# Optimization experiments

Measured on AMD Instinct MI355X. Metric: run time of the kernel, lower is better.

The kernel has to match this reference:

```python
import jax, jax.numpy as jnp
import numpy as np

N = 50000      # nodes
E = 800000     # edges (before self-loops)
IN_DIM = 256
HID = 32       # per-head hidden of conv1
OUT = 8        # per-head out of conv2 (mean over heads)
H = 4          # heads


def setup_inputs() -> dict:
    key = jax.random.key(0)
    k = jax.random.split(key, 8)
    x = jax.random.normal(k[0], (N, IN_DIM), dtype=jnp.float32)
    src = jax.random.randint(k[1], (E,), 0, N)
    dst = jax.random.randint(k[2], (E,), 0, N)
    # emulate remove_self_loops: perturb any accidental self-loop
    dst = jnp.where(src == dst, (dst + 1) % N, dst)
    edge_index = jnp.stack([src, dst])
    sc1 = 1.0 / np.sqrt(IN_DIM)
    W1 = jax.random.uniform(k[3], (IN_DIM, H * HID), jnp.float32, -sc1, sc1)
    att1 = jax.random.uniform(k[4], (H, HID), jnp.float32, -0.1, 0.1)
    b1 = jnp.zeros((H * HID,), jnp.float32)
    sc2 = 1.0 / np.sqrt(H * HID)
    W2 = jax.random.uniform(k[5], (H * HID, H * OUT), jnp.float32, -sc2, sc2)
    att2 = jax.random.uniform(k[6], (H, OUT), jnp.float32, -0.1, 0.1)
    b2 = jnp.zeros((OUT,), jnp.float32)
    return {"x": x, "edge_index": edge_index, "W1": W1, "att1": att1,
            "b1": b1, "W2": W2, "att2": att2, "b2": b2}


def _segment_softmax(logits, seg, num_segments):
    # logits: [E, H], seg: [E] destination ids. Every segment is non-empty
    # (self-loops added), so no -inf survives.
    m = jnp.full((num_segments, logits.shape[1]), -jnp.inf, logits.dtype)
    m = m.at[seg].max(logits)
    e = jnp.exp(logits - m[seg])
    z = jax.ops.segment_sum(e, seg, num_segments=num_segments)
    return e / (z[seg] + 1e-16)


def _oodgat_conv(x, W, att, bias, src, dst, concat):
    n = x.shape[0]
    h = (x @ W).reshape(n, att.shape[0], att.shape[1])          # [N, H, C]
    s = jax.nn.sigmoid(jnp.einsum('nhc,hc->nh', h, att))        # [N, H] node scores
    si, sj = s[dst], s[src]                                      # [E, H]
    # OODGAT similarity weight (adjust=True): agree-in-distribution term
    logits = si * sj + (1.0 - si) * (1.0 - sj)
    alpha = _segment_softmax(logits, dst, n)                     # [E, H]
    msg = h[src] * alpha[:, :, None]                             # [E, H, C]
    out = jax.ops.segment_sum(msg, dst, num_segments=n)          # [N, H, C]
    out = out.reshape(n, -1) if concat else out.mean(axis=1)
    return out + bias


def reference(x, edge_index, W1, att1, b1, W2, att2, b2):
    n = x.shape[0]
    loop = jnp.arange(n)
    src = jnp.concatenate([edge_index[0], loop])  # add_self_loops
    dst = jnp.concatenate([edge_index[1], loop])
    # eval mode: dropout (drop_input/drop_prob/drop_edge) are identity
    h = jax.nn.elu(_oodgat_conv(x, W1, att1, b1, src, dst, True))
    return _oodgat_conv(h, W2, att2, b2, src, dst, False)
```

## Files before the change

kernel.cpp:

```cpp
#include <hip/hip_runtime.h>
#include <math.h>


typedef __attribute__((ext_vector_type(8))) short bf16x8;
typedef __attribute__((ext_vector_type(4))) float f32x4;

__device__ inline ushort f2bf(float f) {
    uint u = __float_as_uint(f);
    return (ushort)((u + 0x7fffu + ((u >> 16) & 1u)) >> 16);
}
__device__ inline float bf_lo(uint u) { return __uint_as_float(u << 16); }
__device__ inline float bf_hi(uint u) { return __uint_as_float(u & 0xffff0000u); }


__global__ void count_pos_k(const int* __restrict__ dstA, int E, int ET,
                            int* __restrict__ deg, ushort* __restrict__ epos) {
    int e = blockIdx.x * blockDim.x + threadIdx.x;
    if (e >= ET) return;
    int d = (e < E) ? dstA[e] : (e - E);
    epos[e] = (ushort)atomicAdd(&deg[d], 1);
}

__global__ __launch_bounds__(256) void scan_a_k(const int* __restrict__ deg, int n,
                                                int* __restrict__ rowstart,
                                                int* __restrict__ bsum) {
    __shared__ int ts[256];
    int t = threadIdx.x;
    int idx = blockIdx.x * 1024 + t * 4;
    int4 v = make_int4(0, 0, 0, 0);
    if (idx + 3 < n) {
        v = *(const int4*)(deg + idx);
    } else {
        if (idx < n)     v.x = deg[idx];
        if (idx + 1 < n) v.y = deg[idx + 1];
        if (idx + 2 < n) v.z = deg[idx + 2];
        if (idx + 3 < n) v.w = deg[idx + 3];
    }
    int s = v.x + v.y + v.z + v.w;
    ts[t] = s;
    __syncthreads();
#pragma unroll
    for (int off = 1; off < 256; off <<= 1) {
        int u = (t >= off) ? ts[t - off] : 0;
        __syncthreads();
        ts[t] += u;
        __syncthreads();
    }
    int excl = ts[t] - s;
    int p1 = excl + v.x, p2 = p1 + v.y, p3 = p2 + v.z;
    if (idx < n)     rowstart[idx]     = excl;
    if (idx + 1 < n) rowstart[idx + 1] = p1;
    if (idx + 2 < n) rowstart[idx + 2] = p2;
    if (idx + 3 < n) rowstart[idx + 3] = p3;
    if (t == 255) bsum[blockIdx.x] = ts[255];
}

__global__ __launch_bounds__(256) void scan_b_k(const int* __restrict__ bsum, int nb,
                                                int* __restrict__ boff,
                                                int* __restrict__ totalp) {
    __shared__ int ts[256];
    int t = threadIdx.x;
    int v = (t < nb) ? bsum[t] : 0;
    ts[t] = v;
    __syncthreads();
#pragma unroll
    for (int off = 1; off < 256; off <<= 1) {
        int u = (t >= off) ? ts[t - off] : 0;
        __syncthreads();
        ts[t] += u;
        __syncthreads();
    }
    if (t < nb) boff[t] = ts[t] - v;
    if (t == nb - 1) *totalp = ts[t];
}

__global__ void scan_c_k(int* __restrict__ rowstart, const int* __restrict__ boff,
                         int n) {
    int i = blockIdx.x * blockDim.x + threadIdx.x;
    if (i < n) rowstart[i] += boff[i >> 10];
}

__global__ void scatter_k(const int* __restrict__ srcA, const int* __restrict__ dstA,
                          int E, int ET, const int* __restrict__ rowstart,
                          const ushort* __restrict__ epos,
                          ushort* __restrict__ csrc) {
    int e = blockIdx.x * blockDim.x + threadIdx.x;
    if (e >= ET) return;
    int d, s;
    if (e < E) { d = dstA[e]; s = srcA[e]; } else { d = e - E; s = e - E; }
    csrc[rowstart[d] + epos[e]] = (ushort)s;
}


__global__ void prep_wt_k(const float* __restrict__ W, ushort* __restrict__ Wt) {
    int idx = blockIdx.x * blockDim.x + threadIdx.x;
    if (idx >= 256 * 128) return;
    int k = idx >> 7, col = idx & 127;
    Wt[col * 256 + k] = f2bf(W[idx]);
}


__global__ __launch_bounds__(256) void gemm1_k(const float* __restrict__ X,
                                               const ushort* __restrict__ Wt,
                                               const float* __restrict__ ATT1,
                                               uint* __restrict__ H1b,
                                               float* __restrict__ S1, int n) {
    __shared__ __align__(16) ushort Alds[4][128][8];
    __shared__ __align__(16) ushort Blds[4][128][8];
    __shared__ float att1s[128];
    int tid = threadIdx.x;
    int wid = tid >> 6;
    int lane = tid & 63;
    int g = lane >> 4;
    int lr = lane & 15;
    int brow = blockIdx.x * 128;
    if (tid < 128) att1s[tid] = ATT1[tid];

    f32x4 acc[2][8];
#pragma unroll
    for (int rt = 0; rt < 2; ++rt)
#pragma unroll
        for (int ct = 0; ct < 8; ++ct) acc[rt][ct] = (f32x4){0.f, 0.f, 0.f, 0.f};

    for (int k0 = 0; k0 < 256; k0 += 32) {
#pragma unroll
        for (int rep = 0; rep < 2; ++rep) {
            int idx = tid + rep * 256;
            int r = idx >> 2, koct = idx & 3;
            int gr = brow + r;
            float4 a0, a1;
            if (gr < n) {
                const float* p = X + (size_t)gr * 256 + k0 + koct * 8;
                a0 = *(const float4*)p;
                a1 = *(const float4*)(p + 4);
            } else {
                a0 = a1 = make_float4(0.f, 0.f, 0.f, 0.f);
            }
            uint4 pk;
            pk.x = (uint)f2bf(a0.x) | ((uint)f2bf(a0.y) << 16);
            pk.y = (uint)f2bf(a0.z) | ((uint)f2bf(a0.w) << 16);
            pk.z = (uint)f2bf(a1.x) | ((uint)f2bf(a1.y) << 16);
            pk.w = (uint)f2bf(a1.z) | ((uint)f2bf(a1.w) << 16);
            *(uint4*)&Alds[koct][r][0] = pk;
        }
#pragma unroll
        for (int rep = 0; rep < 2; ++rep) {
            int idx = tid + rep * 256;
            int col = idx & 127, koct = idx >> 7;
            *(uint4*)&Blds[koct][col][0] =
                *(const uint4*)(Wt + (size_t)col * 256 + k0 + koct * 8);
        }
        __syncthreads();
        bf16x8 xf0 = *(bf16x8*)&Alds[g][wid * 32 + lr][0];
        bf16x8 xf1 = *(bf16x8*)&Alds[g][wid * 32 + 16 + lr][0];
#pragma unroll
        for (int ct = 0; ct < 8; ++ct) {
            bf16x8 wf = *(bf16x8*)&Blds[g][ct * 16 + lr][0];
            acc[0][ct] = __builtin_amdgcn_mfma_f32_16x16x32_bf16(wf, xf0, acc[0][ct], 0, 0, 0);
            acc[1][ct] = __builtin_amdgcn_mfma_f32_16x16x32_bf16(wf, xf1, acc[1][ct], 0, 0, 0);
        }
        __syncthreads();
    }
#pragma unroll
    for (int rt = 0; rt < 2; ++rt) {
        int row = brow + wid * 32 + rt * 16 + lr;
        if (row < n) {
#pragma unroll
            for (int ct = 0; ct < 8; ++ct) {
                uint lo = (uint)f2bf(acc[rt][ct][0]) | ((uint)f2bf(acc[rt][ct][1]) << 16);
                uint hi = (uint)f2bf(acc[rt][ct][2]) | ((uint)f2bf(acc[rt][ct][3]) << 16);
                *(uint2*)(H1b + (size_t)row * 64 + ct * 8 + g * 2) = make_uint2(lo, hi);
            }
        }
        float sc[4] = {0.f, 0.f, 0.f, 0.f};
#pragma unroll
        for (int ct = 0; ct < 8; ++ct) {
            int base = ct * 16 + g * 4;
#pragma unroll
            for (int j = 0; j < 4; ++j)
                sc[ct >> 1] = fmaf(acc[rt][ct][j], att1s[base + j], sc[ct >> 1]);
        }
#pragma unroll
        for (int h = 0; h < 4; ++h) {
            sc[h] += __shfl_xor(sc[h], 16);
            sc[h] += __shfl_xor(sc[h], 32);
        }
        if (g == 0 && row < n) {
            float4 sv;
            sv.x = 1.f / (1.f + __expf(-sc[0]));
            sv.y = 1.f / (1.f + __expf(-sc[1]));
            sv.z = 1.f / (1.f + __expf(-sc[2]));
            sv.w = 1.f / (1.f + __expf(-sc[3]));
            *(float4*)(S1 + (size_t)row * 4) = sv;
        }
    }
}


__global__ __launch_bounds__(512, 8) void conv1_k(const uint* __restrict__ H1b,
                                                  const float* __restrict__ S1,
                                                  const int* __restrict__ rowstart,
                                                  const ushort* __restrict__ csrc,
                                                  const float* __restrict__ b1,
                                                  const float* __restrict__ W2,
                                                  const float* __restrict__ ATT2,
                                                  ushort* __restrict__ H2b,
                                                  float* __restrict__ S2,
                                                  int n, int nwaves) {
    __shared__ float w2t[32][132];
    __shared__ float rowbuf[8][128];
    __shared__ float wbuf[8][64][4];
    __shared__ float att2s[32];
    int tid = threadIdx.x;
    for (int idx = tid; idx < 4096; idx += 512) {
        int k = idx >> 5, c = idx & 31;
        w2t[c][k] = W2[idx];
    }
    if (tid < 32) att2s[tid] = ATT2[tid];
    __syncthreads();

    int wid = tid >> 6;
    int lane = tid & 63;
    int hd = lane >> 4;
    int half = lane >> 5, cc2 = lane & 31;
    int gwave = blockIdx.x * 8 + wid;
    float2 b1v = *(const float2*)(b1 + lane * 2);

    for (int dst = gwave; dst < n; dst += nwaves) {
        int rs = rowstart[dst], re = rowstart[dst + 1];
        float4 si4 = *(const float4*)(S1 + (size_t)dst * 4);
        float z0 = 0.f, z1 = 0.f, z2 = 0.f, z3 = 0.f;
        float x0 = 0.f, x1 = 0.f, x2 = 0.f, x3 = 0.f;
        float y0 = 0.f, y1 = 0.f, y2 = 0.f, y3 = 0.f;

        for (int cb = rs; cb < re; cb += 64) {
            int cc = min(64, re - cb);
            int sv = 0;
            if (lane < cc) {
                sv = csrc[cb + lane];
                float4 sj = *(const float4*)(S1 + (size_t)sv * 4);
                float w0 = __expf(fmaf(si4.x, sj.x, (1.f - si4.x) * (1.f - sj.x)));
                float w1 = __expf(fmaf(si4.y, sj.y, (1.f - si4.y) * (1.f - sj.y)));
                float w2 = __expf(fmaf(si4.z, sj.z, (1.f - si4.z) * (1.f - sj.z)));
                float w3 = __expf(fmaf(si4.w, sj.w, (1.f - si4.w) * (1.f - sj.w)));
                *(float4*)&wbuf[wid][lane][0] = make_float4(w0, w1, w2, w3);
            }
            asm volatile("s_waitcnt lgkmcnt(0)" ::: "memory");
            int e = 0;
            for (; e + 7 < cc; e += 8) {
                int sA = __builtin_amdgcn_readlane(sv, e);
                int sB = __builtin_amdgcn_readlane(sv, e + 1);
                int sC = __builtin_amdgcn_readlane(sv, e + 2);
                int sD = __builtin_amdgcn_readlane(sv, e + 3);
                int sE = __builtin_amdgcn_readlane(sv, e + 4);
                int sF = __builtin_amdgcn_readlane(sv, e + 5);
                int sG = __builtin_amdgcn_readlane(sv, e + 6);
                int sH = __builtin_amdgcn_readlane(sv, e + 7);
                float wA = wbuf[wid][e][hd],     wB = wbuf[wid][e + 1][hd];
                float wC = wbuf[wid][e + 2][hd], wD = wbuf[wid][e + 3][hd];
                float wE = wbuf[wid][e + 4][hd], wF = wbuf[wid][e + 5][hd];
                float wG = wbuf[wid][e + 6][hd], wH = wbuf[wid][e + 7][hd];
                uint uA = H1b[(size_t)sA * 64 + lane];
                uint uB = H1b[(size_t)sB * 64 + lane];
                uint uC = H1b[(size_t)sC * 64 + lane];
                uint uD = H1b[(size_t)sD * 64 + lane];
                uint uE = H1b[(size_t)sE * 64 + lane];
                uint uF = H1b[(size_t)sF * 64 + lane];
                uint uG = H1b[(size_t)sG * 64 + lane];
                uint uH = H1b[(size_t)sH * 64 + lane];
                z0 += wA + wE; z1 += wB + wF; z2 += wC + wG; z3 += wD + wH;
                x0 = fmaf(wA, bf_lo(uA), x0); x1 = fmaf(wB, bf_lo(uB), x1);
                x2 = fmaf(wC, bf_lo(uC), x2); x3 = fmaf(wD, bf_lo(uD), x3);
                x0 = fmaf(wE, bf_lo(uE), x0); x1 = fmaf(wF, bf_lo(uF), x1);
                x2 = fmaf(wG, bf_lo(uG), x2); x3 = fmaf(wH, bf_lo(uH), x3);
                y0 = fmaf(wA, bf_hi(uA), y0); y1 = fmaf(wB, bf_hi(uB), y1);
                y2 = fmaf(wC, bf_hi(uC), y2); y3 = fmaf(wD, bf_hi(uD), y3);
                y0 = fmaf(wE, bf_hi(uE), y0); y1 = fmaf(wF, bf_hi(uF), y1);
                y2 = fmaf(wG, bf_hi(uG), y2); y3 = fmaf(wH, bf_hi(uH), y3);
            }
            for (; e < cc; ++e) {
                int s = __builtin_amdgcn_readlane(sv, e);
                float w = wbuf[wid][e][hd];
                uint u = H1b[(size_t)s * 64 + lane];
                z0 += w;
                x0 = fmaf(w, bf_lo(u), x0);
                y0 = fmaf(w, bf_hi(u), y0);
            }
            asm volatile("" ::: "memory");
        }
        float inv = 1.f / ((z0 + z1) + (z2 + z3) + 1e-16f);
        float r0 = ((x0 + x1) + (x2 + x3)) * inv + b1v.x;
        float r1 = ((y0 + y1) + (y2 + y3)) * inv + b1v.y;
        r0 = (r0 > 0.f) ? r0 : (__expf(r0) - 1.f);
        r1 = (r1 > 0.f) ? r1 : (__expf(r1) - 1.f);

        *(float2*)&rowbuf[wid][lane * 2] = make_float2(r0, r1);
        asm volatile("s_waitcnt lgkmcnt(0)" ::: "memory");
        const float* rb = &rowbuf[wid][half * 64];
        const float* wr = &w2t[cc2][half * 64];
        float sum = 0.f;
#pragma unroll
        for (int k = 0; k < 64; k += 4) {
            float4 rv = *(const float4*)(rb + k);
            float4 wv = *(const float4*)(wr + k);
            sum = fmaf(rv.x, wv.x, sum);
            sum = fmaf(rv.y, wv.y, sum);
            sum = fmaf(rv.z, wv.z, sum);
            sum = fmaf(rv.w, wv.w, sum);
        }
        sum += __shfl_xor(sum, 32);
        if (half == 0) H2b[(size_t)dst * 32 + cc2] = f2bf(sum);

        float v = sum * att2s[cc2];
        v += __shfl_xor(v, 1);
        v += __shfl_xor(v, 2);
        v += __shfl_xor(v, 4);
        if (half == 0 && (cc2 & 7) == 0)
            S2[dst * 4 + (cc2 >> 3)] = 1.f / (1.f + __expf(-v));
    }
}


__global__ __launch_bounds__(256, 8) void conv2_k(const uint* __restrict__ H2u,
                                                  const float* __restrict__ S,
                                                  const int* __restrict__ rowstart,
                                                  const ushort* __restrict__ csrc,
                                                  const float* __restrict__ b2,
                                                  float* __restrict__ Out,
                                                  int n, int nwaves) {
    int gwave = (int)((blockIdx.x * blockDim.x + threadIdx.x) >> 6);
    int lane = threadIdx.x & 63;
    int eslot = lane >> 4;
    int c2 = lane & 15;
    int hd = c2 >> 2;
    float2 b2v;
    b2v.x = b2[2 * (c2 & 3)];
    b2v.y = b2[2 * (c2 & 3) + 1];

    for (int dst = gwave; dst < n; dst += nwaves) {
        float si = S[dst * 4 + hd];
        float omsi = 1.f - si;
        int rs = rowstart[dst], re = rowstart[dst + 1];
        int cnt = re - rs;
        float z = 0.f, x = 0.f, y = 0.f;
        int i = eslot;
        for (; i + 4 < cnt; i += 8) {
            int s0 = csrc[rs + i];
            int s1 = csrc[rs + i + 4];
            float sj0 = S[s0 * 4 + hd];
            float sj1 = S[s1 * 4 + hd];
            uint u0 = H2u[(size_t)s0 * 16 + c2];
            uint u1 = H2u[(size_t)s1 * 16 + c2];
            float w0 = __expf(fmaf(si, sj0, omsi * (1.f - sj0)));
            float w1 = __expf(fmaf(si, sj1, omsi * (1.f - sj1)));
            z += w0 + w1;
            x = fmaf(w0, bf_lo(u0), x); x = fmaf(w1, bf_lo(u1), x);
            y = fmaf(w0, bf_hi(u0), y); y = fmaf(w1, bf_hi(u1), y);
        }
        if (i < cnt) {
            int s0 = csrc[rs + i];
            float sj0 = S[s0 * 4 + hd];
            uint u0 = H2u[(size_t)s0 * 16 + c2];
            float w0 = __expf(fmaf(si, sj0, omsi * (1.f - sj0)));
            z += w0;
            x = fmaf(w0, bf_lo(u0), x);
            y = fmaf(w0, bf_hi(u0), y);
        }
        z += __shfl_xor(z, 16); z += __shfl_xor(z, 32);
        x += __shfl_xor(x, 16); x += __shfl_xor(x, 32);
        y += __shfl_xor(y, 16); y += __shfl_xor(y, 32);
        float inv = 1.f / (z + 1e-16f);
        float r0 = x * inv, r1 = y * inv;
        r0 += __shfl_xor(r0, 4, 16); r0 += __shfl_xor(r0, 8, 16);
        r1 += __shfl_xor(r1, 4, 16); r1 += __shfl_xor(r1, 8, 16);
        if (eslot == 0 && c2 < 4) {
            float2 o = make_float2(r0 * 0.25f + b2v.x, r1 * 0.25f + b2v.y);
            *(float2*)(Out + (size_t)dst * 8 + 2 * c2) = o;
        }
    }
}


static inline size_t align16(size_t x) { return (x + 15) & ~(size_t)15; }

extern "C" void kernel_launch(void* const* d_in, const int* in_sizes, int n_in,
                              void* d_out, int out_size, void* d_ws, size_t ws_size,
                              hipStream_t stream) {
    const float* x    = (const float*)d_in[0];
    const int*   edge = (const int*)d_in[1];
    const float* W1   = (const float*)d_in[2];
    const float* att1 = (const float*)d_in[3];
    const float* b1   = (const float*)d_in[4];
    const float* W2   = (const float*)d_in[5];
    const float* att2 = (const float*)d_in[6];
    const float* b2   = (const float*)d_in[7];

    int N  = in_sizes[0] / 256;
    int E  = in_sizes[1] / 2;
    int ET = E + N;
    int NB = (N + 1023) / 1024;
    const int* srcA = edge;
    const int* dstA = edge + E;

    char* ws = (char*)d_ws;
    uint*  h1b  = (uint*)ws;   ws += align16((size_t)N * 64 * sizeof(uint));
    ushort* h2b = (ushort*)ws; ws += align16((size_t)N * 32 * sizeof(ushort));
    float* s1   = (float*)ws;  ws += align16((size_t)N * 4 * sizeof(float));
    float* s2   = (float*)ws;  ws += align16((size_t)N * 4 * sizeof(float));
    int* rowstart = (int*)ws;  ws += align16((size_t)(N + 1) * sizeof(int));
    int* deg      = (int*)ws;  ws += align16((size_t)N * sizeof(int));
    ushort* csrc  = (ushort*)ws; ws += align16((size_t)ET * sizeof(ushort));
    ushort* epos  = (ushort*)ws; ws += align16((size_t)ET * sizeof(ushort));
    int* bsum     = (int*)ws;  ws += align16((size_t)NB * sizeof(int));
    int* boff     = (int*)ws;  ws += align16((size_t)NB * sizeof(int));
    ushort* w1t   = (ushort*)ws; ws += align16((size_t)256 * 128 * sizeof(ushort));

    hipMemsetAsync(deg, 0, (size_t)N * sizeof(int), stream);

    int eb = (ET + 255) / 256;
    count_pos_k<<<eb, 256, 0, stream>>>(dstA, E, ET, deg, epos);
    scan_a_k<<<NB, 256, 0, stream>>>(deg, N, rowstart, bsum);
    scan_b_k<<<1, 256, 0, stream>>>(bsum, NB, boff, rowstart + N);
    scan_c_k<<<(N + 255) / 256, 256, 0, stream>>>(rowstart, boff, N);
    scatter_k<<<eb, 256, 0, stream>>>(srcA, dstA, E, ET, rowstart, epos, csrc);

    prep_wt_k<<<(256 * 128 + 255) / 256, 256, 0, stream>>>(W1, w1t);
    gemm1_k<<<(N + 127) / 128, 256, 0, stream>>>(x, w1t, att1, h1b, s1, N);

    int c1_blocks = 1024;
    if (c1_blocks > (N + 7) / 8) c1_blocks = (N + 7) / 8;
    int c1_waves = c1_blocks * 8;
    conv1_k<<<c1_blocks, 512, 0, stream>>>(h1b, s1, rowstart, csrc, b1, W2, att2,
                                           h2b, s2, N, c1_waves);

    int c2_blocks = 2048;
    if (c2_blocks > (N + 3) / 4) c2_blocks = (N + 3) / 4;
    int c2_waves = c2_blocks * 4;
    conv2_k<<<c2_blocks, 256, 0, stream>>>((const uint*)h2b, s2, rowstart, csrc, b2,
                                           (float*)d_out, N, c2_waves);
}
```

Baseline: 154.8 us.

## Store conv1 outputs in per-wave slot layout and vectorise CSR build kernels

conv1 now packs each wave's H2 and S2 results into a wave-major slot layout. Two destinations' H2 rows go out in one 32-lane coalesced store, and S2 for four destinations is batched into one 16-lane store, replacing scattered small writes. conv2 remaps node ids to that slot layout with a mask and shift. The count and scatter kernels now process four edges per thread with vectorised index loads. Costs are extra shuffles, index arithmetic in conv2's gather, and a hard-coded wave count of 8192 that ties the layout to the fixed launch and to N ≤ 65536.

```diff
diff --git a/kernel.cpp b/kernel.cpp
--- a/kernel.cpp
+++ b/kernel.cpp
@@ -15,10 +15,26 @@
 
 __global__ void count_pos_k(const int* __restrict__ dstA, int E, int ET,
                             int* __restrict__ deg, ushort* __restrict__ epos) {
-    int e = blockIdx.x * blockDim.x + threadIdx.x;
-    if (e >= ET) return;
-    int d = (e < E) ? dstA[e] : (e - E);
-    epos[e] = (ushort)atomicAdd(&deg[d], 1);
+    int e4 = (blockIdx.x * blockDim.x + threadIdx.x) * 4;
+    if (e4 >= ET) return;
+    if (e4 + 3 < E) {
+        int4 d = *(const int4*)(dstA + e4);
+        ushort4 p;
+        p.x = (ushort)atomicAdd(&deg[d.x], 1);
+        p.y = (ushort)atomicAdd(&deg[d.y], 1);
+        p.z = (ushort)atomicAdd(&deg[d.z], 1);
+        p.w = (ushort)atomicAdd(&deg[d.w], 1);
+        *(ushort4*)(epos + e4) = p;
+    } else {
+#pragma unroll
+        for (int j = 0; j < 4; ++j) {
+            int e = e4 + j;
+            if (e < ET) {
+                int d = (e < E) ? dstA[e] : (e - E);
+                epos[e] = (ushort)atomicAdd(&deg[d], 1);
+            }
+        }
+    }
 }
 
 __global__ __launch_bounds__(256) void scan_a_k(const int* __restrict__ deg, int n,
@@ -84,11 +100,27 @@
                           int E, int ET, const int* __restrict__ rowstart,
                           const ushort* __restrict__ epos,
                           ushort* __restrict__ csrc) {
-    int e = blockIdx.x * blockDim.x + threadIdx.x;
-    if (e >= ET) return;
-    int d, s;
-    if (e < E) { d = dstA[e]; s = srcA[e]; } else { d = e - E; s = e - E; }
-    csrc[rowstart[d] + epos[e]] = (ushort)s;
+    int e4 = (blockIdx.x * blockDim.x + threadIdx.x) * 4;
+    if (e4 >= ET) return;
+    if (e4 + 3 < E) {
+        int4 d = *(const int4*)(dstA + e4);
+        int4 s = *(const int4*)(srcA + e4);
+        ushort4 p = *(const ushort4*)(epos + e4);
+        csrc[rowstart[d.x] + p.x] = (ushort)s.x;
+        csrc[rowstart[d.y] + p.y] = (ushort)s.y;
+        csrc[rowstart[d.z] + p.z] = (ushort)s.z;
+        csrc[rowstart[d.w] + p.w] = (ushort)s.w;
+    } else {
+#pragma unroll
+        for (int j = 0; j < 4; ++j) {
+            int e = e4 + j;
+            if (e < ET) {
+                int d, s;
+                if (e < E) { d = dstA[e]; s = srcA[e]; } else { d = e - E; s = e - E; }
+                csrc[rowstart[d] + epos[e]] = (ushort)s;
+            }
+        }
+    }
 }
 
 
@@ -204,8 +236,8 @@
                                                   const float* __restrict__ b1,
                                                   const float* __restrict__ W2,
                                                   const float* __restrict__ ATT2,
-                                                  ushort* __restrict__ H2b,
-                                                  float* __restrict__ S2,
+                                                  uint* __restrict__ H2p,
+                                                  float* __restrict__ S2p,
                                                   int n, int nwaves) {
     __shared__ float w2t[32][132];
     __shared__ float rowbuf[8][128];
@@ -225,8 +257,12 @@
     int half = lane >> 5, cc2 = lane & 31;
     int gwave = blockIdx.x * 8 + wid;
     float2 b1v = *(const float2*)(b1 + lane * 2);
-
-    for (int dst = gwave; dst < n; dst += nwaves) {
+    float (*wbufw)[4] = wbuf[wid];
+    float* rowbufw = rowbuf[wid];
+
+    float evensum = 0.f, s2pack = 0.f;
+    int i = 0;
+    for (int dst = gwave; dst < n; dst += nwaves, ++i) {
         int rs = rowstart[dst], re = rowstart[dst + 1];
         float4 si4 = *(const float4*)(S1 + (size_t)dst * 4);
         float z0 = 0.f, z1 = 0.f, z2 = 0.f, z3 = 0.f;
@@ -243,7 +279,7 @@
                 float w1 = __expf(fmaf(si4.y, sj.y, (1.f - si4.y) * (1.f - sj.y)));
                 float w2 = __expf(fmaf(si4.z, sj.z, (1.f - si4.z) * (1.f - sj.z)));
                 float w3 = __expf(fmaf(si4.w, sj.w, (1.f - si4.w) * (1.f - sj.w)));
-                *(float4*)&wbuf[wid][lane][0] = make_float4(w0, w1, w2, w3);
+                *(float4*)&wbufw[lane][0] = make_float4(w0, w1, w2, w3);
             }
             asm volatile("s_waitcnt lgkmcnt(0)" ::: "memory");
             int e = 0;
@@ -256,10 +292,10 @@
                 int sF = __builtin_amdgcn_readlane(sv, e + 5);
                 int sG = __builtin_amdgcn_readlane(sv, e + 6);
                 int sH = __builtin_amdgcn_readlane(sv, e + 7);
-                float wA = wbuf[wid][e][hd],     wB = wbuf[wid][e + 1][hd];
-                float wC = wbuf[wid][e + 2][hd], wD = wbuf[wid][e + 3][hd];
-                float wE = wbuf[wid][e + 4][hd], wF = wbuf[wid][e + 5][hd];
-                float wG = wbuf[wid][e + 6][hd], wH = wbuf[wid][e + 7][hd];
+                float wA = wbufw[e][hd],     wB = wbufw[e + 1][hd];
+                float wC = wbufw[e + 2][hd], wD = wbufw[e + 3][hd];
+                float wE = wbufw[e + 4][hd], wF = wbufw[e + 5][hd];
+                float wG = wbufw[e + 6][hd], wH = wbufw[e + 7][hd];
                 uint uA = H1b[(size_t)sA * 64 + lane];
                 uint uB = H1b[(size_t)sB * 64 + lane];
                 uint uC = H1b[(size_t)sC * 64 + lane];
@@ -280,7 +316,7 @@
             }
             for (; e < cc; ++e) {
                 int s = __builtin_amdgcn_readlane(sv, e);
-                float w = wbuf[wid][e][hd];
+                float w = wbufw[e][hd];
                 uint u = H1b[(size_t)s * 64 + lane];
                 z0 += w;
                 x0 = fmaf(w, bf_lo(u), x0);
@@ -294,9 +330,9 @@
         r0 = (r0 > 0.f) ? r0 : (__expf(r0) - 1.f);
         r1 = (r1 > 0.f) ? r1 : (__expf(r1) - 1.f);
 
-        *(float2*)&rowbuf[wid][lane * 2] = make_float2(r0, r1);
+        *(float2*)&rowbufw[lane * 2] = make_float2(r0, r1);
         asm volatile("s_waitcnt lgkmcnt(0)" ::: "memory");
-        const float* rb = &rowbuf[wid][half * 64];
+        const float* rb = &rowbufw[half * 64];
         const float* wr = &w2t[cc2][half * 64];
         float sum = 0.f;
 #pragma unroll
@@ -309,25 +345,53 @@
             sum = fmaf(rv.w, wv.w, sum);
         }
         sum += __shfl_xor(sum, 32);
-        if (half == 0) H2b[(size_t)dst * 32 + cc2] = f2bf(sum);
 
         float v = sum * att2s[cc2];
         v += __shfl_xor(v, 1);
         v += __shfl_xor(v, 2);
         v += __shfl_xor(v, 4);
-        if (half == 0 && (cc2 & 7) == 0)
-            S2[dst * 4 + (cc2 >> 3)] = 1.f / (1.f + __expf(-v));
-    }
-}
-
-
-__global__ __launch_bounds__(256, 8) void conv2_k(const uint* __restrict__ H2u,
-                                                  const float* __restrict__ S,
+
+        float vsrc = __shfl(v, (lane & 3) * 8);
+        if ((lane >> 2) == (i & 3)) s2pack = vsrc;
+        if ((i & 3) == 3 && lane < 16)
+            S2p[(size_t)((gwave << 3) + (i & ~3)) * 4 + lane] =
+                1.f / (1.f + __expf(-s2pack));
+
+        if ((i & 1) == 0) {
+            evensum = sum;
+        } else {
+            int c0 = 2 * (lane & 15);
+            float a = __shfl(evensum, c0), b = __shfl(evensum, c0 + 1);
+            float c = __shfl(sum, c0),     d = __shfl(sum, c0 + 1);
+            uint pk = (lane & 16) ? ((uint)f2bf(c) | ((uint)f2bf(d) << 16))
+                                  : ((uint)f2bf(a) | ((uint)f2bf(b) << 16));
+            if (lane < 32)
+                H2p[(size_t)((gwave << 3) + (i - 1)) * 16 + lane] = pk;
+        }
+    }
+    if (i & 1) {
+        int c0 = 2 * (lane & 15);
+        float a = __shfl(evensum, c0), b = __shfl(evensum, c0 + 1);
+        uint pk = (uint)f2bf(a) | ((uint)f2bf(b) << 16);
+        if (lane < 32)
+            H2p[(size_t)((gwave << 3) + (i - 1)) * 16 + lane] = pk;
+    }
+    if (i & 3) {
+        if (lane < 16)
+            S2p[(size_t)((gwave << 3) + (i & ~3)) * 4 + lane] =
+                1.f / (1.f + __expf(-s2pack));
+    }
+}
+
+
+__global__ __launch_bounds__(256, 8) void conv2_k(const uint* __restrict__ H2p,
+                                                  const float* __restrict__ S2p,
                                                   const int* __restrict__ rowstart,
                                                   const ushort* __restrict__ csrc,
                                                   const float* __restrict__ b2,
                                                   float* __restrict__ Out,
-                                                  int n, int nwaves) {
+                                                  int n, int nwaves2,
+                                                  int c1mask, int c1shift) {
     int gwave = (int)((blockIdx.x * blockDim.x + threadIdx.x) >> 6);
     int lane = threadIdx.x & 63;
     int eslot = lane >> 4;
@@ -337,8 +401,9 @@
     b2v.x = b2[2 * (c2 & 3)];
     b2v.y = b2[2 * (c2 & 3) + 1];
 
-    for (int dst = gwave; dst < n; dst += nwaves) {
-        float si = S[dst * 4 + hd];
+    for (int dst = gwave; dst < n; dst += nwaves2) {
+        int rd = ((dst & c1mask) << 3) | (dst >> c1shift);
+        float si = S2p[(size_t)rd * 4 + hd];
         float omsi = 1.f - si;
         int rs = rowstart[dst], re = rowstart[dst + 1];
         int cnt = re - rs;
@@ -347,10 +412,12 @@
         for (; i + 4 < cnt; i += 8) {
             int s0 = csrc[rs + i];
             int s1 = csrc[rs + i + 4];
-            float sj0 = S[s0 * 4 + hd];
-            float sj1 = S[s1 * 4 + hd];
-            uint u0 = H2u[(size_t)s0 * 16 + c2];
-            uint u1 = H2u[(size_t)s1 * 16 + c2];
+            int r0i = ((s0 & c1mask) << 3) | (s0 >> c1shift);
+            int r1i = ((s1 & c1mask) << 3) | (s1 >> c1shift);
+            float sj0 = S2p[(size_t)r0i * 4 + hd];
+            float sj1 = S2p[(size_t)r1i * 4 + hd];
+            uint u0 = H2p[(size_t)r0i * 16 + c2];
+            uint u1 = H2p[(size_t)r1i * 16 + c2];
             float w0 = __expf(fmaf(si, sj0, omsi * (1.f - sj0)));
             float w1 = __expf(fmaf(si, sj1, omsi * (1.f - sj1)));
             z += w0 + w1;
@@ -359,8 +426,9 @@
         }
         if (i < cnt) {
             int s0 = csrc[rs + i];
-            float sj0 = S[s0 * 4 + hd];
-            uint u0 = H2u[(size_t)s0 * 16 + c2];
+            int r0i = ((s0 & c1mask) << 3) | (s0 >> c1shift);
+            float sj0 = S2p[(size_t)r0i * 4 + hd];
+            uint u0 = H2p[(size_t)r0i * 16 + c2];
             float w0 = __expf(fmaf(si, sj0, omsi * (1.f - sj0)));
             z += w0;
             x = fmaf(w0, bf_lo(u0), x);
@@ -402,40 +470,40 @@
     const int* srcA = edge;
     const int* dstA = edge + E;
 
+    const int C1_WAVES = 8192, C1_MASK = 8191, C1_SHIFT = 13;
+    const int SLOTS = C1_WAVES * 8;
+
     char* ws = (char*)d_ws;
     uint*  h1b  = (uint*)ws;   ws += align16((size_t)N * 64 * sizeof(uint));
-    ushort* h2b = (ushort*)ws; ws += align16((size_t)N * 32 * sizeof(ushort));
+    uint*  h2p  = (uint*)ws;   ws += align16((size_t)SLOTS * 16 * sizeof(uint));
     float* s1   = (float*)ws;  ws += align16((size_t)N * 4 * sizeof(float));
-    float* s2   = (float*)ws;  ws += align16((size_t)N * 4 * sizeof(float));
+    float* s2p  = (float*)ws;  ws += align16((size_t)SLOTS * 4 * sizeof(float));
     int* rowstart = (int*)ws;  ws += align16((size_t)(N + 1) * sizeof(int));
-    int* deg      = (int*)ws;  ws += align16((size_t)N * sizeof(int));
+    size_t degBytes = align16((size_t)N * sizeof(int));
+    int* deg      = (int*)ws;  ws += degBytes;
     ushort* csrc  = (ushort*)ws; ws += align16((size_t)ET * sizeof(ushort));
     ushort* epos  = (ushort*)ws; ws += align16((size_t)ET * sizeof(ushort));
     int* bsum     = (int*)ws;  ws += align16((size_t)NB * sizeof(int));
     int* boff     = (int*)ws;  ws += align16((size_t)NB * sizeof(int));
     ushort* w1t   = (ushort*)ws; ws += align16((size_t)256 * 128 * sizeof(ushort));
 
-    hipMemsetAsync(deg, 0, (size_t)N * sizeof(int), stream);
-
-    int eb = (ET + 255) / 256;
-    count_pos_k<<<eb, 256, 0, stream>>>(dstA, E, ET, deg, epos);
+    hipMemsetAsync(deg, 0, degBytes, stream);
+
+    int eb4 = (ET + 1023) / 1024;
+    count_pos_k<<<eb4, 256, 0, stream>>>(dstA, E, ET, deg, epos);
     scan_a_k<<<NB, 256, 0, stream>>>(deg, N, rowstart, bsum);
     scan_b_k<<<1, 256, 0, stream>>>(bsum, NB, boff, rowstart + N);
     scan_c_k<<<(N + 255) / 256, 256, 0, stream>>>(rowstart, boff, N);
-    scatter_k<<<eb, 256, 0, stream>>>(srcA, dstA, E, ET, rowstart, epos, csrc);
+    scatter_k<<<eb4, 256, 0, stream>>>(srcA, dstA, E, ET, rowstart, epos, csrc);
 
     prep_wt_k<<<(256 * 128 + 255) / 256, 256, 0, stream>>>(W1, w1t);
     gemm1_k<<<(N + 127) / 128, 256, 0, stream>>>(x, w1t, att1, h1b, s1, N);
 
-    int c1_blocks = 1024;
-    if (c1_blocks > (N + 7) / 8) c1_blocks = (N + 7) / 8;
-    int c1_waves = c1_blocks * 8;
-    conv1_k<<<c1_blocks, 512, 0, stream>>>(h1b, s1, rowstart, csrc, b1, W2, att2,
-                                           h2b, s2, N, c1_waves);
+    conv1_k<<<1024, 512, 0, stream>>>(h1b, s1, rowstart, csrc, b1, W2, att2,
+                                      h2p, s2p, N, C1_WAVES);
 
     int c2_blocks = 2048;
-    if (c2_blocks > (N + 3) / 4) c2_blocks = (N + 3) / 4;
-    int c2_waves = c2_blocks * 4;
-    conv2_k<<<c2_blocks, 256, 0, stream>>>((const uint*)h2b, s2, rowstart, csrc, b2,
-                                           (float*)d_out, N, c2_waves);
-}
+    conv2_k<<<c2_blocks, 256, 0, stream>>>(h2p, s2p, rowstart, csrc, b2,
+                                           (float*)d_out, N, c2_blocks * 4,
+                                           C1_MASK, C1_SHIFT);
+}
```

New measurement: 161.7 us. +4.5%, slower.
